# Kernel optimization log

Hardware: AMD Instinct MI355X
Metric: run time of the kernel (lower is better)

## Reference

```python
import jax, jax.numpy as jnp
import numpy as np
import math

LMAX = 5
TAU_PRE = 16
TAU = 16
B = 256


def _cg_coeff(l1, l2, l, m1, m2, m):
    # Standard Clebsch-Gordan coefficient <l1 m1 l2 m2 | l m> (Racah formula).
    if m1 + m2 != m or l < abs(l1 - l2) or l > l1 + l2:
        return 0.0
    f = math.factorial
    pref = math.sqrt((2 * l + 1) * f(l + l1 - l2) * f(l - l1 + l2) * f(l1 + l2 - l) / f(l1 + l2 + l + 1))
    pref *= math.sqrt(f(l + m) * f(l - m) * f(l1 - m1) * f(l1 + m1) * f(l2 - m2) * f(l2 + m2))
    kmin = max(0, l2 - l - m1, l1 + m2 - l)
    kmax = min(l1 + l2 - l, l1 - m1, l2 + m2)
    s = 0.0
    for k in range(kmin, kmax + 1):
        s += (-1) ** k / (f(k) * f(l1 + l2 - l - k) * f(l1 - m1 - k) * f(l2 + m2 - k) * f(l - l2 + m1 + k) * f(l - l1 - m2 + k))
    return pref * s


def _build_cg(lmax):
    # Enumerate (l1, l2<=l1, l) triples exactly as UpdateFunction._calculate_number_of_cols / fCG do.
    triples, tensors = [], {}
    for l1 in range(lmax + 1):
        for l2 in range(l1 + 1):
            for l in range(abs(l1 - l2), min(l1 + l2 + 1, lmax + 1)):
                C = np.zeros((2 * l + 1, 2 * l1 + 1, 2 * l2 + 1), dtype=np.float32)
                for m in range(-l, l + 1):
                    for m1 in range(-l1, l1 + 1):
                        m2 = m - m1
                        if -l2 <= m2 <= l2:
                            C[m + l, m1 + l1, m2 + l2] = _cg_coeff(l1, l2, l, m1, m2, m)
                triples.append((l1, l2, l))
                tensors[(l1, l2, l)] = jnp.asarray(C)
    return triples, tensors


TRIPLES, CG = _build_cg(LMAX)
NUMCOLS = [sum(TAU_PRE * TAU_PRE for (_, _, l) in TRIPLES if l == L) for L in range(LMAX + 1)]


def _cg_transform(fs):
    # CG tensor product: for each (l1,l2,l) triple form complex channel-pair products
    # contracted with CG coefficients; concat fragments along the channel axis per l.
    frags = [[] for _ in range(LMAX + 1)]
    for (l1, l2, l) in TRIPLES:
        C = CG[(l1, l2, l)]                       # [2l+1, 2l1+1, 2l2+1]
        f1, f2 = fs[l1], fs[l2]                   # [B, t, 2l*+1, 2]
        f1r, f1i = f1[..., 0], f1[..., 1]
        f2r, f2i = f2[..., 0], f2[..., 1]
        rr = jnp.einsum('kmn,bim,bjn->bijk', C, f1r, f2r)
        ii = jnp.einsum('kmn,bim,bjn->bijk', C, f1i, f2i)
        ri = jnp.einsum('kmn,bim,bjn->bijk', C, f1r, f2i)
        ir = jnp.einsum('kmn,bim,bjn->bijk', C, f1i, f2r)
        frag = jnp.stack([rr - ii, ri + ir], axis=-1)          # [B, t1, t2, 2l+1, 2]
        bsz = f1.shape[0]
        frags[l].append(frag.reshape(bsz, -1, 2 * l + 1, 2))
    return [jnp.concatenate(fl, axis=1) for fl in frags]       # per l: [B, numcols[l], 2l+1, 2]


def _complex_mm(w, f):
    # Complex_bmm with w broadcast over the batch: w [tau, cols, 2], f [B, cols, 2l+1, 2].
    wr, wi = w[..., 0], w[..., 1]
    fr, fi = f[..., 0], f[..., 1]
    real = jnp.einsum('tc,bck->btk', wr, fr) - jnp.einsum('tc,bck->btk', wi, fi)
    imag = jnp.einsum('tc,bck->btk', wr, fi) + jnp.einsum('tc,bck->btk', wi, fr)
    return jnp.stack([real, imag], axis=-1)                    # [B, tau, 2l+1, 2]


def setup_inputs() -> dict:
    key = jax.random.key(0)
    inp = {}
    for l in range(LMAX + 1):
        inp['f%d' % l] = jax.random.normal(jax.random.fold_in(key, l), (B, TAU_PRE, 2 * l + 1, 2), dtype=jnp.float32)
        inp['w%d' % l] = 0.05 * jax.random.uniform(jax.random.fold_in(key, 100 + l), (TAU, NUMCOLS[l], 2), dtype=jnp.float32)
    return inp


def reference(f0, f1, f2, f3, f4, f5, w0, w1, w2, w3, w4, w5):
    fs = [f0, f1, f2, f3, f4, f5]
    ws = [w0, w1, w2, w3, w4, w5]
    new_fs = _cg_transform(fs)
    return tuple(_complex_mm(ws[l], new_fs[l]) for l in range(LMAX + 1))
```

## Files before the change

kernel.cpp:

```cpp
#include <hip/hip_runtime.h>
#include <hip/hip_fp16.h>
#include <utility>


using f32x4 = __attribute__((ext_vector_type(4))) float;
using f16x8 = __attribute__((ext_vector_type(8))) _Float16;

constexpr int OUTOFF_[6]  = {0, 8192, 32768, 73728, 131072, 204800};
constexpr int NUMCOLS_[6] = {1536, 2560, 3328, 3584, 3584, 3072};
constexpr int FOFFH_[6]   = {0, 16, 64, 144, 256, 400};
constexpr int WOFF_[6]    = {0, 49152, 131072, 237568, 352256, 466944};

constexpr int TRI_N[6] = {6, 10, 13, 14, 14, 12};
constexpr int TRI_L1[6][14] = {
    {0,1,2,3,4,5, 0,0,0,0,0,0,0,0},
    {1,1,2,2,3,3,4,4,5,5, 0,0,0,0},
    {1,2,2,2,3,3,3,4,4,4,5,5,5, 0},
    {2,2,3,3,3,3,4,4,4,4,5,5,5,5},
    {2,3,3,3,4,4,4,4,4,5,5,5,5,5},
    {3,3,4,4,4,4,5,5,5,5,5,5, 0,0}};
constexpr int TRI_L2[6][14] = {
    {0,1,2,3,4,5, 0,0,0,0,0,0,0,0},
    {0,1,1,2,2,3,3,4,4,5, 0,0,0,0},
    {1,0,1,2,1,2,3,2,3,4,3,4,5, 0},
    {1,2,0,1,2,3,1,2,3,4,2,3,4,5},
    {2,1,2,3,0,1,2,3,4,1,2,3,4,5},
    {2,3,1,2,3,4,0,1,2,3,4,5, 0,0}};

constexpr double cfact(int n) { double r = 1.0; for (int i = 2; i <= n; ++i) r *= (double)i; return r; }

constexpr double csqrt(double x) {
    if (x <= 0.0) return 0.0;
    double g = x < 1.0 ? 1.0 : x;
    for (int i = 0; i < 200; ++i) {
        double n = 0.5 * (g + x / g);
        if (n == g) break;
        g = n;
    }
    return g;
}

constexpr double cg_c(int l1, int l2, int l, int m1, int m2, int m) {
    double pref = (2.0 * l + 1.0) * cfact(l + l1 - l2) * cfact(l - l1 + l2) *
                  cfact(l1 + l2 - l) / cfact(l1 + l2 + l + 1);
    pref *= cfact(l + m) * cfact(l - m) * cfact(l1 - m1) * cfact(l1 + m1) *
            cfact(l2 - m2) * cfact(l2 + m2);
    pref = csqrt(pref);
    int kmin = 0;
    if (l2 - l - m1 > kmin) kmin = l2 - l - m1;
    if (l1 + m2 - l > kmin) kmin = l1 + m2 - l;
    int kmax = l1 + l2 - l;
    if (l1 - m1 < kmax) kmax = l1 - m1;
    if (l2 + m2 < kmax) kmax = l2 + m2;
    double s = 0.0;
    for (int k = kmin; k <= kmax; ++k) {
        double d = cfact(k) * cfact(l1 + l2 - l - k) * cfact(l1 - m1 - k) *
                   cfact(l2 + m2 - k) * cfact(l - l2 + m1 + k) * cfact(l - l1 - m2 + k);
        s += ((k & 1) ? -1.0 : 1.0) / d;
    }
    return pref * s;
}

template <int L1, int L2, int L>
struct CGTab {
    static constexpr int N1 = 2 * L1 + 1, N2 = 2 * L2 + 1;
    struct T { float v[N1 * N2]; };
    static constexpr T build() {
        T t{};
        for (int m1 = -L1; m1 <= L1; ++m1)
            for (int m2 = -L2; m2 <= L2; ++m2) {
                int m = m1 + m2;
                double v = 0.0;
                if (m >= -L && m <= L) v = cg_c(L1, L2, L, m1, m2, m);
                t.v[(m1 + L1) * N2 + (m2 + L2)] = (float)v;
            }
        return t;
    }
    static constexpr T TAB = build();
};

__global__ __launch_bounds__(256)
void wconv_kernel(const float* __restrict__ w0, const float* __restrict__ w1,
                  const float* __restrict__ w2, const float* __restrict__ w3,
                  const float* __restrict__ w4, const float* __restrict__ w5,
                  unsigned short* __restrict__ dst)
{
    const int l = blockIdx.y;
    const float* srcs[6] = {w0, w1, w2, w3, w4, w5};
    const float* src = srcs[l];
    const int cnt = 16 * NUMCOLS_[l] * 2;
    const int i4 = (blockIdx.x * 256 + threadIdx.x) * 4;
    if (i4 < cnt) {
        const float4 v = *(const float4*)(src + i4);
        __half hx = __float2half(v.x), hy = __float2half(v.y);
        __half hz = __float2half(v.z), hw = __float2half(v.w);
        ushort4 o;
        o.x = *(unsigned short*)&hx; o.y = *(unsigned short*)&hy;
        o.z = *(unsigned short*)&hz; o.w = *(unsigned short*)&hw;
        *(ushort4*)(dst + WOFF_[l] + i4) = o;
    }
}

template <int L, int L1, int L2>
__device__ __forceinline__ void do_phase1(const unsigned* __restrict__ sh_fh,
                                          char* __restrict__ frag, const int tid)
{
    constexpr int N1 = 2 * L1 + 1, N2 = 2 * L2 + 1, NK = 2 * L + 1, SH = L1 + L2 - L;
    const int i = tid >> 4, j = tid & 15;
    const unsigned* f1 = sh_fh + FOFFH_[L1] + i * N1;
    const unsigned* f2 = sh_fh + FOFFH_[L2] + j * N2;

    unsigned axx[N1], ayy[N1], bv[N2], bsn[N2];
#pragma unroll
    for (int m = 0; m < N1; ++m) {
        const unsigned a = f1[m];
        const unsigned lo = a & 0xffffu, hi = a >> 16;
        axx[m] = lo | (lo << 16);
        ayy[m] = hi | (hi << 16);
    }
#pragma unroll
    for (int n = 0; n < N2; ++n) {
        const unsigned b = f2[n];
        bv[n] = b;
        bsn[n] = ((b >> 16) | (b << 16)) ^ 0x8000u;
    }

    const int ij4 = tid * 4;
#pragma unroll
    for (int k = 0; k < NK; ++k) {
        const int kk = k + SH;
        __half2 acc = __float2half2_rn(0.0f);
#pragma unroll
        for (int m1 = 0; m1 < N1; ++m1) {
            const int m2 = kk - m1;
            if (m2 >= 0 && m2 < N2) {
                const float c = CGTab<L1, L2, L>::TAB.v[m1 * N2 + m2];
                if (c != 0.f) {
                    const __half2 p = __hfma2(*(const __half2*)&ayy[m1],
                                              *(const __half2*)&bsn[m2],
                                              __hmul2(*(const __half2*)&axx[m1],
                                                      *(const __half2*)&bv[m2]));
                    acc = __hfma2(__float2half2_rn(c), p, acc);
                }
            }
        }
        *(__half2*)(frag + ((k * 1024 + ij4) ^ ((k & 7) << 4))) = acc;
    }
}

template <int L>
__device__ __forceinline__ void do_mfma(const char* __restrict__ frag,
                                        const unsigned short* __restrict__ wh,
                                        const int cbase, const int wave,
                                        const int lane, f32x4& PR, f32x4& PI)
{
    constexpr int NK = 2 * L + 1;
    const int t = lane & 15, g = lane >> 4;
    int nc = lane & 15; if (nc > NK - 1) nc = NK - 1;
    const int C = NUMCOLS_[L];
#pragma unroll
    for (int ks = 0; ks < 4; ++ks) {
        const int c0 = wave * 64 + ks * 16 + 4 * g;
        uint4 wa = *(const uint4*)(wh + (size_t)(t * C + cbase + c0) * 2);
        uint4 a1, a2;
        a1.x = wa.x ^ 0x80000000u; a1.y = wa.y ^ 0x80000000u;
        a1.z = wa.z ^ 0x80000000u; a1.w = wa.w ^ 0x80000000u;
        a2.x = (wa.x >> 16) | (wa.x << 16); a2.y = (wa.y >> 16) | (wa.y << 16);
        a2.z = (wa.z >> 16) | (wa.z << 16); a2.w = (wa.w >> 16) | (wa.w << 16);
        const int byt = (nc * 1024 + c0 * 4) ^ ((nc & 7) << 4);
        const f16x8 B = *(const f16x8*)(frag + byt);
        PR = __builtin_amdgcn_mfma_f32_16x16x32_f16(*(const f16x8*)&a1, B, PR, 0, 0, 0);
        PI = __builtin_amdgcn_mfma_f32_16x16x32_f16(*(const f16x8*)&a2, B, PI, 0, 0, 0);
    }
}

template <int L, int IDX>
__device__ __forceinline__ void step(const unsigned* sh_fh, char* frag,
                                     const unsigned short* wh, const int tid,
                                     const int wave, const int lane,
                                     f32x4& PR, f32x4& PI)
{
    do_phase1<L, TRI_L1[L][IDX], TRI_L2[L][IDX]>(sh_fh, frag, tid);
    do_mfma<L>(frag, wh, IDX * 256, wave, lane, PR, PI);
    __builtin_amdgcn_sched_barrier(0);
}

template <int L, int... Is>
__device__ __forceinline__ void run_steps(std::integer_sequence<int, Is...>,
    const unsigned* sh_fh, char* frag, const unsigned short* wh,
    int tid, int wave, int lane, f32x4& PR, f32x4& PI)
{
    (step<L, Is>(sh_fh, frag, wh, tid, wave, lane, PR, PI), ...);
}

template <int L>
__device__ void run_l(const float* const* fs, const unsigned short* __restrict__ wh,
                      float* __restrict__ out, unsigned* sh_fh, char* frag, float* pb)
{
    const int b = blockIdx.x, tid = threadIdx.x;
    const int wave = tid >> 6, lane = tid & 63;

#pragma unroll
    for (int l = 0; l < 6; ++l) {
        const int cnt = 16 * (2 * l + 1);
        const float2* s2 = (const float2*)(fs[l] + (size_t)b * 32 * (2 * l + 1));
        if (tid < cnt) {
            const float2 v = s2[tid];
            const __half2 h = __floats2half2_rn(v.x, v.y);
            sh_fh[FOFFH_[l] + tid] = *(const unsigned*)&h;
        }
    }
    __syncthreads();

    f32x4 PR = {0.f, 0.f, 0.f, 0.f}, PI = {0.f, 0.f, 0.f, 0.f};

    run_steps<L>(std::make_integer_sequence<int, TRI_N[L]>{},
                 sh_fh, frag, wh, tid, wave, lane, PR, PI);

    constexpr int NK = 2 * L + 1;
    {
        const int kcol = lane & 15, g = lane >> 4;
#pragma unroll
        for (int r = 0; r < 4; ++r) {
            pb[(wave * 2 + 0) * 256 + (4 * g + r) * 16 + kcol] = PR[r];
            pb[(wave * 2 + 1) * 256 + (4 * g + r) * 16 + kcol] = PI[r];
        }
    }
    __syncthreads();

    if (tid < 16 * NK) {
        const int t = tid & 15, k = tid >> 4;
        float oR = 0.f, oI = 0.f;
#pragma unroll
        for (int w = 0; w < 4; ++w) {
            oR += pb[(w * 2 + 0) * 256 + t * 16 + k];
            oI += pb[(w * 2 + 1) * 256 + t * 16 + k];
        }
        float* op = out + OUTOFF_[L] + ((size_t)(b * 16 + t) * NK + k) * 2;
        op[0] = oR;
        op[1] = oI;
    }
}

__global__ __launch_bounds__(256, 4)
void update_kernel(const float* __restrict__ f0, const float* __restrict__ f1,
                   const float* __restrict__ f2, const float* __restrict__ f3,
                   const float* __restrict__ f4, const float* __restrict__ f5,
                   const unsigned short* __restrict__ wh,
                   float* __restrict__ out)
{
    __shared__ unsigned sh_fh[576];
    __shared__ __align__(16) char frag[11264];
    __shared__ __align__(16) float pb[2048];
    const float* fs[6] = {f0, f1, f2, f3, f4, f5};
    switch (blockIdx.y) {
        case 0: run_l<5>(fs, wh + WOFF_[5], out, sh_fh, frag, pb); break;
        case 1: run_l<4>(fs, wh + WOFF_[4], out, sh_fh, frag, pb); break;
        case 2: run_l<3>(fs, wh + WOFF_[3], out, sh_fh, frag, pb); break;
        case 3: run_l<2>(fs, wh + WOFF_[2], out, sh_fh, frag, pb); break;
        case 4: run_l<1>(fs, wh + WOFF_[1], out, sh_fh, frag, pb); break;
        default: run_l<0>(fs, wh + WOFF_[0], out, sh_fh, frag, pb); break;
    }
}

extern "C" void kernel_launch(void* const* d_in, const int* in_sizes, int n_in,
                              void* d_out, int out_size, void* d_ws, size_t ws_size,
                              hipStream_t stream)
{
    const float* f[6];
    const float* w[6];
    for (int l = 0; l < 6; ++l) {
        f[l] = (const float*)d_in[2 * l];
        w[l] = (const float*)d_in[2 * l + 1];
    }
    unsigned short* wh = (unsigned short*)d_ws;

    wconv_kernel<<<dim3(112, 6), dim3(256), 0, stream>>>(
        w[0], w[1], w[2], w[3], w[4], w[5], wh);

    update_kernel<<<dim3(256, 6), dim3(256), 0, stream>>>(
        f[0], f[1], f[2], f[3], f[4], f[5], wh, (float*)d_out);
}
```

Baseline: 112.5 us.

## Precompute negated and swapped fp16 weight planes; hoist per-thread feature unpacking to registers

The weight conversion kernel now writes two fp16 planes, one with the imaginary part negated and one with real and imaginary swapped. The MFMA loop loads them directly instead of applying xor and rotate on each load. The per-thread f1/f2 feature values for all l are unpacked from shared memory once into register arrays rather than reloaded in every triple step, and the occupancy hint drops from 4 to 3 blocks to make room for the extra registers. In exchange, the update kernel reads twice as many weight bytes and register pressure rises.

Measured after the change: 149.7 us. 33.0% more time.

```diff
diff --git a/kernel.cpp b/kernel.cpp
--- a/kernel.cpp
+++ b/kernel.cpp
@@ -9,7 +9,9 @@
 constexpr int OUTOFF_[6]  = {0, 8192, 32768, 73728, 131072, 204800};
 constexpr int NUMCOLS_[6] = {1536, 2560, 3328, 3584, 3584, 3072};
 constexpr int FOFFH_[6]   = {0, 16, 64, 144, 256, 400};
-constexpr int WOFF_[6]    = {0, 49152, 131072, 237568, 352256, 466944};
+constexpr int WOFFC_[6]   = {0, 24576, 65536, 118784, 176128, 233472};
+constexpr int WTOT_C      = 282624;
+constexpr int CF_[6]      = {0, 1, 4, 9, 16, 25};
 
 constexpr int TRI_N[6] = {6, 10, 13, 14, 14, 12};
 constexpr int TRI_L1[6][14] = {
@@ -83,45 +85,39 @@
 void wconv_kernel(const float* __restrict__ w0, const float* __restrict__ w1,
                   const float* __restrict__ w2, const float* __restrict__ w3,
                   const float* __restrict__ w4, const float* __restrict__ w5,
-                  unsigned short* __restrict__ dst)
+                  unsigned* __restrict__ a1dst, unsigned* __restrict__ a2dst)
 {
     const int l = blockIdx.y;
     const float* srcs[6] = {w0, w1, w2, w3, w4, w5};
     const float* src = srcs[l];
-    const int cnt = 16 * NUMCOLS_[l] * 2;
-    const int i4 = (blockIdx.x * 256 + threadIdx.x) * 4;
-    if (i4 < cnt) {
-        const float4 v = *(const float4*)(src + i4);
-        __half hx = __float2half(v.x), hy = __float2half(v.y);
-        __half hz = __float2half(v.z), hw = __float2half(v.w);
-        ushort4 o;
-        o.x = *(unsigned short*)&hx; o.y = *(unsigned short*)&hy;
-        o.z = *(unsigned short*)&hz; o.w = *(unsigned short*)&hw;
-        *(ushort4*)(dst + WOFF_[l] + i4) = o;
+    const int cntc = 16 * NUMCOLS_[l];
+    const int ic = (blockIdx.x * 256 + threadIdx.x) * 2;
+    if (ic < cntc) {
+        const float4 v = *(const float4*)(src + ic * 2);
+        const __half2 p0 = __floats2half2_rn(v.x, -v.y);
+        const __half2 p1 = __floats2half2_rn(v.z, -v.w);
+        const __half2 q0 = __floats2half2_rn(v.y, v.x);
+        const __half2 q1 = __floats2half2_rn(v.w, v.z);
+        uint2 o1, o2;
+        o1.x = *(const unsigned*)&p0; o1.y = *(const unsigned*)&p1;
+        o2.x = *(const unsigned*)&q0; o2.y = *(const unsigned*)&q1;
+        *(uint2*)(a1dst + WOFFC_[l] + ic) = o1;
+        *(uint2*)(a2dst + WOFFC_[l] + ic) = o2;
     }
 }
 
 template <int L, int L1, int L2>
-__device__ __forceinline__ void do_phase1(const unsigned* __restrict__ sh_fh,
+__device__ __forceinline__ void do_phase1(const unsigned (&axxc)[36],
+                                          const unsigned (&ayyc)[36],
+                                          const unsigned (&f2c)[36],
                                           char* __restrict__ frag, const int tid)
 {
     constexpr int N1 = 2 * L1 + 1, N2 = 2 * L2 + 1, NK = 2 * L + 1, SH = L1 + L2 - L;
-    const int i = tid >> 4, j = tid & 15;
-    const unsigned* f1 = sh_fh + FOFFH_[L1] + i * N1;
-    const unsigned* f2 = sh_fh + FOFFH_[L2] + j * N2;
-
-    unsigned axx[N1], ayy[N1], bv[N2], bsn[N2];
-#pragma unroll
-    for (int m = 0; m < N1; ++m) {
-        const unsigned a = f1[m];
-        const unsigned lo = a & 0xffffu, hi = a >> 16;
-        axx[m] = lo | (lo << 16);
-        ayy[m] = hi | (hi << 16);
-    }
+
+    unsigned bsn[N2];
 #pragma unroll
     for (int n = 0; n < N2; ++n) {
-        const unsigned b = f2[n];
-        bv[n] = b;
+        const unsigned b = f2c[CF_[L2] + n];
         bsn[n] = ((b >> 16) | (b << 16)) ^ 0x8000u;
     }
 
@@ -136,10 +132,10 @@
             if (m2 >= 0 && m2 < N2) {
                 const float c = CGTab<L1, L2, L>::TAB.v[m1 * N2 + m2];
                 if (c != 0.f) {
-                    const __half2 p = __hfma2(*(const __half2*)&ayy[m1],
+                    const __half2 p = __hfma2(*(const __half2*)&ayyc[CF_[L1] + m1],
                                               *(const __half2*)&bsn[m2],
-                                              __hmul2(*(const __half2*)&axx[m1],
-                                                      *(const __half2*)&bv[m2]));
+                                              __hmul2(*(const __half2*)&axxc[CF_[L1] + m1],
+                                                      *(const __half2*)&f2c[CF_[L2] + m2]));
                     acc = __hfma2(__float2half2_rn(c), p, acc);
                 }
             }
@@ -150,7 +146,8 @@
 
 template <int L>
 __device__ __forceinline__ void do_mfma(const char* __restrict__ frag,
-                                        const unsigned short* __restrict__ wh,
+                                        const unsigned* __restrict__ wA1,
+                                        const unsigned* __restrict__ wA2,
                                         const int cbase, const int wave,
                                         const int lane, f32x4& PR, f32x4& PI)
 {
@@ -161,12 +158,9 @@
 #pragma unroll
     for (int ks = 0; ks < 4; ++ks) {
         const int c0 = wave * 64 + ks * 16 + 4 * g;
-        uint4 wa = *(const uint4*)(wh + (size_t)(t * C + cbase + c0) * 2);
-        uint4 a1, a2;
-        a1.x = wa.x ^ 0x80000000u; a1.y = wa.y ^ 0x80000000u;
-        a1.z = wa.z ^ 0x80000000u; a1.w = wa.w ^ 0x80000000u;
-        a2.x = (wa.x >> 16) | (wa.x << 16); a2.y = (wa.y >> 16) | (wa.y << 16);
-        a2.z = (wa.z >> 16) | (wa.z << 16); a2.w = (wa.w >> 16) | (wa.w << 16);
+        const int off = t * C + cbase + c0;
+        const uint4 a1 = *(const uint4*)(wA1 + off);
+        const uint4 a2 = *(const uint4*)(wA2 + off);
         const int byt = (nc * 1024 + c0 * 4) ^ ((nc & 7) << 4);
         const f16x8 B = *(const f16x8*)(frag + byt);
         PR = __builtin_amdgcn_mfma_f32_16x16x32_f16(*(const f16x8*)&a1, B, PR, 0, 0, 0);
@@ -175,30 +169,34 @@
 }
 
 template <int L, int IDX>
-__device__ __forceinline__ void step(const unsigned* sh_fh, char* frag,
-                                     const unsigned short* wh, const int tid,
-                                     const int wave, const int lane,
+__device__ __forceinline__ void step(const unsigned (&axxc)[36], const unsigned (&ayyc)[36],
+                                     const unsigned (&f2c)[36], char* frag,
+                                     const unsigned* wA1, const unsigned* wA2,
+                                     const int tid, const int wave, const int lane,
                                      f32x4& PR, f32x4& PI)
 {
-    do_phase1<L, TRI_L1[L][IDX], TRI_L2[L][IDX]>(sh_fh, frag, tid);
-    do_mfma<L>(frag, wh, IDX * 256, wave, lane, PR, PI);
+    do_phase1<L, TRI_L1[L][IDX], TRI_L2[L][IDX]>(axxc, ayyc, f2c, frag, tid);
+    do_mfma<L>(frag, wA1, wA2, IDX * 256, wave, lane, PR, PI);
     __builtin_amdgcn_sched_barrier(0);
 }
 
 template <int L, int... Is>
 __device__ __forceinline__ void run_steps(std::integer_sequence<int, Is...>,
-    const unsigned* sh_fh, char* frag, const unsigned short* wh,
+    const unsigned (&axxc)[36], const unsigned (&ayyc)[36], const unsigned (&f2c)[36],
+    char* frag, const unsigned* wA1, const unsigned* wA2,
     int tid, int wave, int lane, f32x4& PR, f32x4& PI)
 {
-    (step<L, Is>(sh_fh, frag, wh, tid, wave, lane, PR, PI), ...);
+    (step<L, Is>(axxc, ayyc, f2c, frag, wA1, wA2, tid, wave, lane, PR, PI), ...);
 }
 
 template <int L>
-__device__ void run_l(const float* const* fs, const unsigned short* __restrict__ wh,
+__device__ void run_l(const float* const* fs,
+                      const unsigned* __restrict__ wA1, const unsigned* __restrict__ wA2,
                       float* __restrict__ out, unsigned* sh_fh, char* frag, float* pb)
 {
     const int b = blockIdx.x, tid = threadIdx.x;
     const int wave = tid >> 6, lane = tid & 63;
+    const int i = tid >> 4, j = tid & 15;
 
 #pragma unroll
     for (int l = 0; l < 6; ++l) {
@@ -212,10 +210,25 @@
     }
     __syncthreads();
 
+    unsigned axxc[36], ayyc[36], f2c[36];
+#pragma unroll
+    for (int l = 0; l < 6; ++l) {
+        const int n = 2 * l + 1;
+#pragma unroll
+        for (int m = 0; m < n; ++m) {
+            const unsigned a = sh_fh[FOFFH_[l] + i * n + m];
+            const unsigned lo = a & 0xffffu;
+            axxc[CF_[l] + m] = lo | (lo << 16);
+            const unsigned hi = a >> 16;
+            ayyc[CF_[l] + m] = hi | (hi << 16);
+            f2c[CF_[l] + m] = sh_fh[FOFFH_[l] + j * n + m];
+        }
+    }
+
     f32x4 PR = {0.f, 0.f, 0.f, 0.f}, PI = {0.f, 0.f, 0.f, 0.f};
 
     run_steps<L>(std::make_integer_sequence<int, TRI_N[L]>{},
-                 sh_fh, frag, wh, tid, wave, lane, PR, PI);
+                 axxc, ayyc, f2c, frag, wA1, wA2, tid, wave, lane, PR, PI);
 
     constexpr int NK = 2 * L + 1;
     {
@@ -242,11 +255,11 @@
     }
 }
 
-__global__ __launch_bounds__(256, 4)
+__global__ __launch_bounds__(256, 3)
 void update_kernel(const float* __restrict__ f0, const float* __restrict__ f1,
                    const float* __restrict__ f2, const float* __restrict__ f3,
                    const float* __restrict__ f4, const float* __restrict__ f5,
-                   const unsigned short* __restrict__ wh,
+                   const unsigned* __restrict__ wA1, const unsigned* __restrict__ wA2,
                    float* __restrict__ out)
 {
     __shared__ unsigned sh_fh[576];
@@ -254,12 +267,12 @@
     __shared__ __align__(16) float pb[2048];
     const float* fs[6] = {f0, f1, f2, f3, f4, f5};
     switch (blockIdx.y) {
-        case 0: run_l<5>(fs, wh + WOFF_[5], out, sh_fh, frag, pb); break;
-        case 1: run_l<4>(fs, wh + WOFF_[4], out, sh_fh, frag, pb); break;
-        case 2: run_l<3>(fs, wh + WOFF_[3], out, sh_fh, frag, pb); break;
-        case 3: run_l<2>(fs, wh + WOFF_[2], out, sh_fh, frag, pb); break;
-        case 4: run_l<1>(fs, wh + WOFF_[1], out, sh_fh, frag, pb); break;
-        default: run_l<0>(fs, wh + WOFF_[0], out, sh_fh, frag, pb); break;
+        case 0: run_l<5>(fs, wA1 + WOFFC_[5], wA2 + WOFFC_[5], out, sh_fh, frag, pb); break;
+        case 1: run_l<4>(fs, wA1 + WOFFC_[4], wA2 + WOFFC_[4], out, sh_fh, frag, pb); break;
+        case 2: run_l<3>(fs, wA1 + WOFFC_[3], wA2 + WOFFC_[3], out, sh_fh, frag, pb); break;
+        case 3: run_l<2>(fs, wA1 + WOFFC_[2], wA2 + WOFFC_[2], out, sh_fh, frag, pb); break;
+        case 4: run_l<1>(fs, wA1 + WOFFC_[1], wA2 + WOFFC_[1], out, sh_fh, frag, pb); break;
+        default: run_l<0>(fs, wA1 + WOFFC_[0], wA2 + WOFFC_[0], out, sh_fh, frag, pb); break;
     }
 }
 
@@ -273,11 +286,12 @@
         f[l] = (const float*)d_in[2 * l];
         w[l] = (const float*)d_in[2 * l + 1];
     }
-    unsigned short* wh = (unsigned short*)d_ws;
+    unsigned* wA1 = (unsigned*)d_ws;
+    unsigned* wA2 = wA1 + WTOT_C;
 
     wconv_kernel<<<dim3(112, 6), dim3(256), 0, stream>>>(
-        w[0], w[1], w[2], w[3], w[4], w[5], wh);
+        w[0], w[1], w[2], w[3], w[4], w[5], wA1, wA2);
 
     update_kernel<<<dim3(256, 6), dim3(256), 0, stream>>>(
-        f[0], f[1], f[2], f[3], f[4], f[5], wh, (float*)d_out);
-}
+        f[0], f[1], f[2], f[3], f[4], f[5], wA1, wA2, (float*)d_out);
+}
```
